# Optimization experiments

Measured on AMD Instinct MI355X. Metric: run time of the kernel, lower is better.

## Reference

```python
import jax, jax.numpy as jnp
import numpy as np

NUM_HEADS = 8
EPS = 1e-6


def _edge_boost(x, density_weight):
    # x: [B, C, H, W] -> boost: [B, H*W] (per-query additive bias)
    B, C, H, W = x.shape
    sx = jnp.array([[-1., 0., 1.], [-2., 0., 2.], [-1., 0., 1.]], dtype=x.dtype)
    sy = jnp.array([[-1., -2., -1.], [0., 0., 0.], [1., 2., 1.]], dtype=x.dtype)
    feat_mean = x.mean(axis=1, keepdims=True)            # [B,1,H,W]
    kern = jnp.stack([sx, sy])[:, None]                  # [2,1,3,3] (OIHW)
    g = jax.lax.conv_general_dilated(
        feat_mean, kern, window_strides=(1, 1), padding='SAME',
        dimension_numbers=('NCHW', 'OIHW', 'NCHW'))     # [B,2,H,W]
    edge = jnp.sqrt(g[:, 0] ** 2 + g[:, 1] ** 2 + EPS)   # [B,H,W]
    return density_weight * jnp.log1p(edge.reshape(B, H * W))


def setup_inputs() -> dict:
    key = jax.random.key(0)
    k1, k2, k3 = jax.random.split(key, 3)
    B, C, H, W = 2, 256, 56, 56
    x = jax.random.normal(k1, (B, C, H, W), dtype=jnp.float32)
    Wqkv = jax.random.normal(k2, (3 * C, C), dtype=jnp.float32) * 0.02
    Wproj = jax.random.normal(k3, (C, C), dtype=jnp.float32) * 0.02
    bproj = jnp.zeros((C,), dtype=jnp.float32)
    density_weight = jnp.float32(1.0)
    return {"x": x, "Wqkv": Wqkv, "Wproj": Wproj, "bproj": bproj,
            "density_weight": density_weight}


def reference(x, Wqkv, Wproj, bproj, density_weight):
    B, C, H, W = x.shape
    h = NUM_HEADS
    d = C // h
    N = H * W
    scale = d ** -0.5

    x_flat = x.reshape(B, C, N).transpose(0, 2, 1)        # [B,N,C]
    qkv = x_flat @ Wqkv.T                                 # [B,N,3C]
    qkv = qkv.reshape(B, N, 3, h, d).transpose(2, 0, 3, 1, 4)  # [3,B,h,N,d]
    q, k, v = qkv[0], qkv[1], qkv[2]

    attn = jnp.einsum('bhqd,bhkd->bhqk', q, k) * scale    # [B,h,N,N]
    boost = _edge_boost(x, density_weight)                # [B,N]
    attn = attn + boost[:, None, :, None]                 # per-query bias, bcast over heads/keys
    attn = jax.nn.softmax(attn, axis=-1)
    # dropout is identity in eval mode

    out = jnp.einsum('bhqk,bhkd->bhqd', attn, v)          # [B,h,N,d]
    out = out.transpose(0, 2, 1, 3).reshape(B, N, C)      # [B,N,C]
    out = out @ Wproj.T + bproj
    return out.transpose(0, 2, 1).reshape(B, C, H, W)
```

## Files before the change

### kernel.cpp

```cpp
#include <hip/hip_runtime.h>
#include <hip/hip_bf16.h>
#include <math.h>

#define NQ    3136
#define CDIM  256
#define HEADS 8
#define NT    49


typedef __attribute__((ext_vector_type(8))) short short8;
typedef __attribute__((ext_vector_type(4))) float f32x4;

__device__ __forceinline__ short f2bf(float f) {
    union { float f; unsigned u; } v; v.f = f;
    unsigned r = v.u + 0x7fff + ((v.u >> 16) & 1);
    return (short)(r >> 16);
}

__device__ __forceinline__ unsigned pk_bf16(float a, float b) {
    unsigned r;
    asm("v_cvt_pk_bf16_f32 %0, %1, %2" : "=v"(r) : "v"(a), "v"(b));
    return r;
}

#define SCALE_L2E 0.25503487523f

__global__ __launch_bounds__(256) void prep(const float* __restrict__ x,
                                            const float* __restrict__ Wq,
                                            const float* __restrict__ Wp,
                                            short* __restrict__ xT,
                                            short* __restrict__ Wb,
                                            short* __restrict__ Wpb) {
    const int bx = blockIdx.x;
    const int t  = threadIdx.x;
    if (bx == 52) {
        const int wp   = blockIdx.y + 4 * blockIdx.z;
        const int base = wp * 8192 + t * 4;
        #pragma unroll
        for (int i = 0; i < 8; ++i) {
            float4 v = *(const float4*)(Wp + base + i * 1024);
            uint2 o = { pk_bf16(v.x, v.y), pk_bf16(v.z, v.w) };
            *(uint2*)(Wpb + base + i * 1024) = o;
        }
        return;
    }
    if (bx >= 49) {
        const int wb   = (bx - 49) + 3 * (blockIdx.y + 4 * blockIdx.z);
        const int base = wb * 8192 + t * 4;
        #pragma unroll
        for (int i = 0; i < 8; ++i) {
            float4 v = *(const float4*)(Wq + base + i * 1024);
            uint2 o = { pk_bf16(v.x, v.y), pk_bf16(v.z, v.w) };
            *(uint2*)(Wb + base + i * 1024) = o;
        }
        return;
    }
    __shared__ short lt[64][72];
    const int b = blockIdx.z, cb = blockIdx.y, nb = bx;
    const float* xb = x + (size_t)b * CDIM * NQ + (size_t)(cb * 64) * NQ + nb * 64;
    #pragma unroll
    for (int it = 0; it < 4; ++it) {
        const int cc = (t >> 4) + 16 * it;
        const int nn = (t & 15) * 4;
        float4 v = *(const float4*)(xb + (size_t)cc * NQ + nn);
        lt[nn + 0][cc] = f2bf(v.x);
        lt[nn + 1][cc] = f2bf(v.y);
        lt[nn + 2][cc] = f2bf(v.z);
        lt[nn + 3][cc] = f2bf(v.w);
    }
    __syncthreads();
    const int n2 = t >> 2, c2 = (t & 3) * 16;
    short* dst = xT + ((size_t)b * NQ + nb * 64 + n2) * CDIM + cb * 64 + c2;
    *(uint4*)dst       = *(const uint4*)&lt[n2][c2];
    *(uint4*)(dst + 8) = *(const uint4*)&lt[n2][c2 + 8];
}

__global__ __launch_bounds__(256) void qkv_mfma(const short* __restrict__ xT,
                                                const short* __restrict__ Wb,
                                                short* __restrict__ Qs,
                                                short* __restrict__ Kb,
                                                short* __restrict__ V4) {
    __shared__ short xs[64][40];
    __shared__ short wsm[64][40];
    __shared__ short eps[64][72];
    const int nb = blockIdx.x, jb = blockIdx.y, b = blockIdx.z;
    const int n0 = nb * 64, j0 = jb * 64;
    const int t = threadIdx.x;
    const int lane = t & 63, w = t >> 6, g = lane >> 4, ql = lane & 15;
    const int srow = t >> 2, sc = (t & 3) * 8;

    const short* xsrc = xT + ((size_t)b * NQ + n0 + srow) * CDIM + sc;
    const short* wsrc = Wb + (size_t)(j0 + srow) * CDIM + sc;

    short8 xr = *(const short8*)(xsrc);
    short8 wr = *(const short8*)(wsrc);

    f32x4 acc[4] = {};
    for (int c0 = 0; c0 < 256; c0 += 32) {
        *(short8*)&xs[srow][sc]  = xr;
        *(short8*)&wsm[srow][sc] = wr;
        __syncthreads();
        if (c0 + 32 < 256) {
            xr = *(const short8*)(xsrc + c0 + 32);
            wr = *(const short8*)(wsrc + c0 + 32);
        }
        short8 bf = *(const short8*)&wsm[16 * w + ql][8 * g];
        #pragma unroll
        for (int r = 0; r < 4; ++r) {
            short8 af = *(const short8*)&xs[16 * r + ql][8 * g];
            acc[r] = __builtin_amdgcn_mfma_f32_16x16x32_bf16(af, bf, acc[r], 0, 0, 0);
        }
        __syncthreads();
    }

    const int sect = jb >> 2;
    const int hb   = (jb & 3) * 2;
    const int jloc = 16 * w + ql;

    if (sect < 2) {
        const float sc2 = (sect == 0) ? SCALE_L2E : 1.0f;
        #pragma unroll
        for (int r = 0; r < 4; ++r)
            #pragma unroll
            for (int i = 0; i < 4; ++i)
                eps[16 * r + 4 * g + i][jloc] = f2bf(acc[r][i] * sc2);
        __syncthreads();
        short* dstb = (sect == 0) ? Qs : Kb;
        const int n2 = t >> 2, jc = (t & 3) * 16;
        const int head = hb + (jc >> 5), d0 = jc & 31;
        short* dst = dstb + ((size_t)(b * 8 + head) * NQ + n0 + n2) * 32 + d0;
        *(uint4*)dst       = *(const uint4*)&eps[n2][jc];
        *(uint4*)(dst + 8) = *(const uint4*)&eps[n2][jc + 8];
    } else {
        #pragma unroll
        for (int r = 0; r < 4; ++r)
            #pragma unroll
            for (int i = 0; i < 4; ++i)
                eps[jloc][16 * r + 4 * g + i] = f2bf(acc[r][i]);
        __syncthreads();
        const int f  = t >> 6;
        const int l2 = t & 63;
        const int gg = l2 >> 4, qq = l2 & 15;
        const int dl = ((f & 2) ? 16 : 0) + qq;
        const int ko = ((f & 1) ? 32 : 0) + 8 * gg;
        #pragma unroll
        for (int h2 = 0; h2 < 2; ++h2) {
            const uint4 val = *(const uint4*)&eps[32 * h2 + dl][ko];
            short* dst = V4 + ((((size_t)(b * 8 + hb + h2) * NT + nb) * 4 + f) * 64 + l2) * 8;
            *(uint4*)dst = val;
        }
    }
}

__global__ __launch_bounds__(256) void attn_mfma(const short* __restrict__ Qs,
                                                 const short* __restrict__ Kb,
                                                 const short* __restrict__ V4,
                                                 short* __restrict__ Ob) {
    __shared__ __align__(16) short pq[4][32][72];

    const int bid = blockIdx.x;
    const int xcd = bid & 7;
    const int ii  = bid >> 3;
    const int bh  = xcd * 2 + (ii & 1);
    const int q0  = (ii >> 1) * 32;

    const int t    = threadIdx.x;
    const int lane = t & 63;
    const int w    = t >> 6;
    const int g    = lane >> 4;
    const int ql   = lane & 15;

    const short* Qh = Qs + (size_t)bh * NQ * 32;
    const short* Kh = Kb + (size_t)bh * NQ * 32;
    const short* Vh = V4 + (size_t)bh * (NT * 2048) + (size_t)lane * 8;

    const short8 qfA = *(const short8*)(Qh + (size_t)(q0 + ql) * 32 + 8 * g);
    const short8 qfB = *(const short8*)(Qh + (size_t)(q0 + 16 + ql) * 32 + 8 * g);

    short8 ones;
    #pragma unroll
    for (int e = 0; e < 8; ++e) ones[e] = (short)0x3F80;

    const short* kp = Kh + (size_t)ql * 32 + 8 * g;

    f32x4 otA0 = {0,0,0,0}, otA1 = {0,0,0,0};
    f32x4 otB0 = {0,0,0,0}, otB1 = {0,0,0,0};
    f32x4 otlA = {0,0,0,0}, otlB = {0,0,0,0};

    const short* vt0 = Vh + (size_t)w * 2048;
    short8 vc00 = *(const short8*)(vt0);
    short8 vc01 = *(const short8*)(vt0 + 512);
    short8 vc10 = *(const short8*)(vt0 + 1024);
    short8 vc11 = *(const short8*)(vt0 + 1536);

    for (int i = 0; i < 13; ++i) {
        const int cur = 4 * i + w;
        const int nxt = cur + 4;
        const int tn  = (nxt < NT) ? nxt : w;
        const short* vtn = Vh + (size_t)tn * 2048;
        short8 vn00 = *(const short8*)(vtn);
        short8 vn01 = *(const short8*)(vtn + 512);
        short8 vn10 = *(const short8*)(vtn + 1024);
        short8 vn11 = *(const short8*)(vtn + 1536);

        if (cur < NT) {
            const int k0 = cur * 64;
            short8 kf0 = *(const short8*)(kp + (size_t)(k0 +  0) * 32);
            short8 kf1 = *(const short8*)(kp + (size_t)(k0 + 16) * 32);
            short8 kf2 = *(const short8*)(kp + (size_t)(k0 + 32) * 32);
            short8 kf3 = *(const short8*)(kp + (size_t)(k0 + 48) * 32);

            __builtin_amdgcn_s_setprio(1);
            f32x4 stA[4], stB[4];
            stA[0] = __builtin_amdgcn_mfma_f32_16x16x32_bf16(kf0, qfA, (f32x4){0,0,0,0}, 0, 0, 0);
            stB[0] = __builtin_amdgcn_mfma_f32_16x16x32_bf16(kf0, qfB, (f32x4){0,0,0,0}, 0, 0, 0);
            stA[1] = __builtin_amdgcn_mfma_f32_16x16x32_bf16(kf1, qfA, (f32x4){0,0,0,0}, 0, 0, 0);
            stB[1] = __builtin_amdgcn_mfma_f32_16x16x32_bf16(kf1, qfB, (f32x4){0,0,0,0}, 0, 0, 0);
            stA[2] = __builtin_amdgcn_mfma_f32_16x16x32_bf16(kf2, qfA, (f32x4){0,0,0,0}, 0, 0, 0);
            stB[2] = __builtin_amdgcn_mfma_f32_16x16x32_bf16(kf2, qfB, (f32x4){0,0,0,0}, 0, 0, 0);
            stA[3] = __builtin_amdgcn_mfma_f32_16x16x32_bf16(kf3, qfA, (f32x4){0,0,0,0}, 0, 0, 0);
            stB[3] = __builtin_amdgcn_mfma_f32_16x16x32_bf16(kf3, qfB, (f32x4){0,0,0,0}, 0, 0, 0);
            __builtin_amdgcn_s_setprio(0);

            float pA[16], pB[16];
            #pragma unroll
            for (int c = 0; c < 4; ++c)
                #pragma unroll
                for (int e = 0; e < 4; ++e) {
                    pA[4 * c + e] = __builtin_amdgcn_exp2f(stA[c][e]);
                    pB[4 * c + e] = __builtin_amdgcn_exp2f(stB[c][e]);
                }

            #pragma unroll
            for (int c = 0; c < 4; ++c) {
                uint2 va_ = { pk_bf16(pA[4 * c + 0], pA[4 * c + 1]),
                              pk_bf16(pA[4 * c + 2], pA[4 * c + 3]) };
                *(uint2*)&pq[w][ql][16 * c + 4 * g] = va_;
                uint2 vb_ = { pk_bf16(pB[4 * c + 0], pB[4 * c + 1]),
                              pk_bf16(pB[4 * c + 2], pB[4 * c + 3]) };
                *(uint2*)&pq[w][16 + ql][16 * c + 4 * g] = vb_;
            }
            asm volatile("s_waitcnt lgkmcnt(0)" ::: "memory");

            short8 pbA0 = *(const short8*)&pq[w][ql][8 * g];
            short8 pbA1 = *(const short8*)&pq[w][ql][32 + 8 * g];
            short8 pbB0 = *(const short8*)&pq[w][16 + ql][8 * g];
            short8 pbB1 = *(const short8*)&pq[w][16 + ql][32 + 8 * g];

            __builtin_amdgcn_s_setprio(1);
            otA0 = __builtin_amdgcn_mfma_f32_16x16x32_bf16(vc00, pbA0, otA0, 0, 0, 0);
            otA0 = __builtin_amdgcn_mfma_f32_16x16x32_bf16(vc01, pbA1, otA0, 0, 0, 0);
            otA1 = __builtin_amdgcn_mfma_f32_16x16x32_bf16(vc10, pbA0, otA1, 0, 0, 0);
            otA1 = __builtin_amdgcn_mfma_f32_16x16x32_bf16(vc11, pbA1, otA1, 0, 0, 0);
            otB0 = __builtin_amdgcn_mfma_f32_16x16x32_bf16(vc00, pbB0, otB0, 0, 0, 0);
            otB0 = __builtin_amdgcn_mfma_f32_16x16x32_bf16(vc01, pbB1, otB0, 0, 0, 0);
            otB1 = __builtin_amdgcn_mfma_f32_16x16x32_bf16(vc10, pbB0, otB1, 0, 0, 0);
            otB1 = __builtin_amdgcn_mfma_f32_16x16x32_bf16(vc11, pbB1, otB1, 0, 0, 0);
            otlA = __builtin_amdgcn_mfma_f32_16x16x32_bf16(ones, pbA0, otlA, 0, 0, 0);
            otlA = __builtin_amdgcn_mfma_f32_16x16x32_bf16(ones, pbA1, otlA, 0, 0, 0);
            otlB = __builtin_amdgcn_mfma_f32_16x16x32_bf16(ones, pbB0, otlB, 0, 0, 0);
            otlB = __builtin_amdgcn_mfma_f32_16x16x32_bf16(ones, pbB1, otlB, 0, 0, 0);
            __builtin_amdgcn_s_setprio(0);
        }

        vc00 = vn00; vc01 = vn01; vc10 = vn10; vc11 = vn11;
    }

    const float lA = otlA[0];
    const float lB = otlB[0];

    __syncthreads();
    float* mrg = (float*)&pq[0][0][0];
    if (w > 0) {
        float* pp = mrg + ((size_t)(w - 1) * 64 + lane) * 20;
        *(f32x4*)(pp + 0)  = otA0;
        *(f32x4*)(pp + 4)  = otA1;
        *(f32x4*)(pp + 8)  = otB0;
        *(f32x4*)(pp + 12) = otB1;
        pp[16] = lA; pp[17] = lB;
    }
    __syncthreads();
    if (w == 0) {
        f32x4 sA0 = otA0, sA1 = otA1, sB0 = otB0, sB1 = otB1;
        float LA = lA, LB = lB;
        #pragma unroll
        for (int u = 0; u < 3; ++u) {
            const float* pp = mrg + ((size_t)u * 64 + lane) * 20;
            sA0 += *(const f32x4*)(pp + 0);
            sA1 += *(const f32x4*)(pp + 4);
            sB0 += *(const f32x4*)(pp + 8);
            sB1 += *(const f32x4*)(pp + 12);
            LA += pp[16]; LB += pp[17];
        }
        const float invA = 1.f / LA;
        const float invB = 1.f / LB;
        const int b = bh >> 3, h = bh & 7;
        short* orowA = Ob + ((size_t)b * NQ + q0 + ql) * CDIM + h * 32;
        short* orowB = Ob + ((size_t)b * NQ + q0 + 16 + ql) * CDIM + h * 32;
        uint2 wA0 = { pk_bf16(sA0[0] * invA, sA0[1] * invA),
                      pk_bf16(sA0[2] * invA, sA0[3] * invA) };
        uint2 wA1 = { pk_bf16(sA1[0] * invA, sA1[1] * invA),
                      pk_bf16(sA1[2] * invA, sA1[3] * invA) };
        uint2 wB0 = { pk_bf16(sB0[0] * invB, sB0[1] * invB),
                      pk_bf16(sB0[2] * invB, sB0[3] * invB) };
        uint2 wB1 = { pk_bf16(sB1[0] * invB, sB1[1] * invB),
                      pk_bf16(sB1[2] * invB, sB1[3] * invB) };
        *(uint2*)(orowA + 4 * g)      = wA0;
        *(uint2*)(orowA + 16 + 4 * g) = wA1;
        *(uint2*)(orowB + 4 * g)      = wB0;
        *(uint2*)(orowB + 16 + 4 * g) = wB1;
    }
}

__global__ __launch_bounds__(256) void proj_mfma(const short* __restrict__ Ob,
                                                 const short* __restrict__ Wpb,
                                                 const float* __restrict__ bias,
                                                 float* __restrict__ out) {
    __shared__ short xs[32][40];
    __shared__ short wsm[64][40];
    __shared__ float eps[64][36];
    const int n0  = blockIdx.x * 32;
    const int co0 = blockIdx.y * 64;
    const int b   = blockIdx.z;
    const int t   = threadIdx.x;
    const int lane = t & 63, w = t >> 6, g = lane >> 4, ql = lane & 15;
    const int arow = (t & 127) >> 2, ac = (t & 3) * 8;
    const int brow = t >> 2,          bc = (t & 3) * 8;

    const short* asrc = Ob + ((size_t)b * NQ + n0 + arow) * CDIM + ac;
    const short* wsrc = Wpb + (size_t)(co0 + brow) * CDIM + bc;

    short8 ar = {};
    if (t < 128) ar = *(const short8*)(asrc);
    short8 wr = *(const short8*)(wsrc);

    f32x4 acc0 = {}, acc1 = {};
    for (int c0 = 0; c0 < 256; c0 += 32) {
        if (t < 128) *(short8*)&xs[arow][ac] = ar;
        *(short8*)&wsm[brow][bc] = wr;
        __syncthreads();
        if (c0 + 32 < 256) {
            if (t < 128) ar = *(const short8*)(asrc + c0 + 32);
            wr = *(const short8*)(wsrc + c0 + 32);
        }
        short8 bfr = *(const short8*)&wsm[16 * w + ql][8 * g];
        short8 af0 = *(const short8*)&xs[ql][8 * g];
        short8 af1 = *(const short8*)&xs[16 + ql][8 * g];
        acc0 = __builtin_amdgcn_mfma_f32_16x16x32_bf16(af0, bfr, acc0, 0, 0, 0);
        acc1 = __builtin_amdgcn_mfma_f32_16x16x32_bf16(af1, bfr, acc1, 0, 0, 0);
        __syncthreads();
    }

    const int jl = 16 * w + ql;
    const float bb = bias[co0 + jl];
    *(float4*)&eps[jl][4 * g]      = make_float4(acc0[0] + bb, acc0[1] + bb,
                                                 acc0[2] + bb, acc0[3] + bb);
    *(float4*)&eps[jl][16 + 4 * g] = make_float4(acc1[0] + bb, acc1[1] + bb,
                                                 acc1[2] + bb, acc1[3] + bb);
    __syncthreads();

    const int row = t >> 2, seg = (t & 3) * 8;
    float* outp = out + ((size_t)b * CDIM + co0 + row) * NQ + n0 + seg;
    *(float4*)(outp)     = *(const float4*)&eps[row][seg];
    *(float4*)(outp + 4) = *(const float4*)&eps[row][seg + 4];
}

extern "C" void kernel_launch(void* const* d_in, const int* in_sizes, int n_in,
                              void* d_out, int out_size, void* d_ws, size_t ws_size,
                              hipStream_t stream) {
    const float* x     = (const float*)d_in[0];
    const float* Wqkv  = (const float*)d_in[1];
    const float* Wproj = (const float*)d_in[2];
    const float* bproj = (const float*)d_in[3];
    float* out = (float*)d_out;

    short* xT  = (short*)d_ws;
    short* Wb  = xT + (size_t)2 * NQ * CDIM;
    short* Wpb = Wb + (size_t)768 * CDIM;
    short* Qs  = Wpb + (size_t)CDIM * CDIM;
    short* Kb  = Qs + (size_t)16 * NQ * 32;
    short* V4  = Kb + (size_t)16 * NQ * 32;
    short* Ob  = V4 + (size_t)16 * NT * 2048;

    prep<<<dim3(53, 4, 2), 256, 0, stream>>>(x, Wqkv, Wproj, xT, Wb, Wpb);
    qkv_mfma<<<dim3(49, 12, 2), 256, 0, stream>>>(xT, Wb, Qs, Kb, V4);
    attn_mfma<<<dim3(1568, 1, 1), 256, 0, stream>>>(Qs, Kb, V4, Ob);
    proj_mfma<<<dim3(98, 4, 2), 256, 0, stream>>>(Ob, Wpb, bproj, out);
}
```

Before: 66.48 us.

## Widen attention blocks to 64 queries and 7 waves with tree reduction

Each attention block now handles 64 queries instead of 32, so every K and V tile loaded into registers is reused for four query sub-tiles rather than two. The key split grows from 4 to 7 waves (448 threads), so the 49 key tiles divide evenly and the per-iteration bounds check goes away. The grid is halved to match. The cross-wave merge of partial outputs and row sums becomes a multi-step tree reduction through a larger shared buffer. In exchange, register pressure and LDS use per block rise, there are more barriers, and with fewer, larger blocks occupancy and wave scheduling may get worse.

```diff
diff --git a/kernel.cpp b/kernel.cpp
--- a/kernel.cpp
+++ b/kernel.cpp
@@ -152,17 +152,17 @@
     }
 }
 
-__global__ __launch_bounds__(256) void attn_mfma(const short* __restrict__ Qs,
+__global__ __launch_bounds__(448) void attn_mfma(const short* __restrict__ Qs,
                                                  const short* __restrict__ Kb,
                                                  const short* __restrict__ V4,
                                                  short* __restrict__ Ob) {
-    __shared__ __align__(16) short pq[4][32][72];
+    __shared__ __align__(16) short pq[7][32][72];
 
     const int bid = blockIdx.x;
     const int xcd = bid & 7;
     const int ii  = bid >> 3;
     const int bh  = xcd * 2 + (ii & 1);
-    const int q0  = (ii >> 1) * 32;
+    const int q0  = (ii >> 1) * 64;
 
     const int t    = threadIdx.x;
     const int lane = t & 63;
@@ -176,6 +176,8 @@
 
     const short8 qfA = *(const short8*)(Qh + (size_t)(q0 + ql) * 32 + 8 * g);
     const short8 qfB = *(const short8*)(Qh + (size_t)(q0 + 16 + ql) * 32 + 8 * g);
+    const short8 qfC = *(const short8*)(Qh + (size_t)(q0 + 32 + ql) * 32 + 8 * g);
+    const short8 qfD = *(const short8*)(Qh + (size_t)(q0 + 48 + ql) * 32 + 8 * g);
 
     short8 ones;
     #pragma unroll
@@ -185,7 +187,10 @@
 
     f32x4 otA0 = {0,0,0,0}, otA1 = {0,0,0,0};
     f32x4 otB0 = {0,0,0,0}, otB1 = {0,0,0,0};
+    f32x4 otC0 = {0,0,0,0}, otC1 = {0,0,0,0};
+    f32x4 otD0 = {0,0,0,0}, otD1 = {0,0,0,0};
     f32x4 otlA = {0,0,0,0}, otlB = {0,0,0,0};
+    f32x4 otlC = {0,0,0,0}, otlD = {0,0,0,0};
 
     const short* vt0 = Vh + (size_t)w * 2048;
     short8 vc00 = *(const short8*)(vt0);
@@ -193,9 +198,9 @@
     short8 vc10 = *(const short8*)(vt0 + 1024);
     short8 vc11 = *(const short8*)(vt0 + 1536);
 
-    for (int i = 0; i < 13; ++i) {
-        const int cur = 4 * i + w;
-        const int nxt = cur + 4;
+    for (int i = 0; i < 7; ++i) {
+        const int cur = 7 * i + w;
+        const int nxt = cur + 7;
         const int tn  = (nxt < NT) ? nxt : w;
         const short* vtn = Vh + (size_t)tn * 2048;
         short8 vn00 = *(const short8*)(vtn);
@@ -203,13 +208,13 @@
         short8 vn10 = *(const short8*)(vtn + 1024);
         short8 vn11 = *(const short8*)(vtn + 1536);
 
-        if (cur < NT) {
-            const int k0 = cur * 64;
-            short8 kf0 = *(const short8*)(kp + (size_t)(k0 +  0) * 32);
-            short8 kf1 = *(const short8*)(kp + (size_t)(k0 + 16) * 32);
-            short8 kf2 = *(const short8*)(kp + (size_t)(k0 + 32) * 32);
-            short8 kf3 = *(const short8*)(kp + (size_t)(k0 + 48) * 32);
-
+        const int k0 = cur * 64;
+        short8 kf0 = *(const short8*)(kp + (size_t)(k0 +  0) * 32);
+        short8 kf1 = *(const short8*)(kp + (size_t)(k0 + 16) * 32);
+        short8 kf2 = *(const short8*)(kp + (size_t)(k0 + 32) * 32);
+        short8 kf3 = *(const short8*)(kp + (size_t)(k0 + 48) * 32);
+
+        {
             __builtin_amdgcn_s_setprio(1);
             f32x4 stA[4], stB[4];
             stA[0] = __builtin_amdgcn_mfma_f32_16x16x32_bf16(kf0, qfA, (f32x4){0,0,0,0}, 0, 0, 0);
@@ -230,7 +235,6 @@
                     pA[4 * c + e] = __builtin_amdgcn_exp2f(stA[c][e]);
                     pB[4 * c + e] = __builtin_amdgcn_exp2f(stB[c][e]);
                 }
-
             #pragma unroll
             for (int c = 0; c < 4; ++c) {
                 uint2 va_ = { pk_bf16(pA[4 * c + 0], pA[4 * c + 1]),
@@ -263,53 +267,123 @@
             __builtin_amdgcn_s_setprio(0);
         }
 
+        {
+            __builtin_amdgcn_s_setprio(1);
+            f32x4 stC[4], stD[4];
+            stC[0] = __builtin_amdgcn_mfma_f32_16x16x32_bf16(kf0, qfC, (f32x4){0,0,0,0}, 0, 0, 0);
+            stD[0] = __builtin_amdgcn_mfma_f32_16x16x32_bf16(kf0, qfD, (f32x4){0,0,0,0}, 0, 0, 0);
+            stC[1] = __builtin_amdgcn_mfma_f32_16x16x32_bf16(kf1, qfC, (f32x4){0,0,0,0}, 0, 0, 0);
+            stD[1] = __builtin_amdgcn_mfma_f32_16x16x32_bf16(kf1, qfD, (f32x4){0,0,0,0}, 0, 0, 0);
+            stC[2] = __builtin_amdgcn_mfma_f32_16x16x32_bf16(kf2, qfC, (f32x4){0,0,0,0}, 0, 0, 0);
+            stD[2] = __builtin_amdgcn_mfma_f32_16x16x32_bf16(kf2, qfD, (f32x4){0,0,0,0}, 0, 0, 0);
+            stC[3] = __builtin_amdgcn_mfma_f32_16x16x32_bf16(kf3, qfC, (f32x4){0,0,0,0}, 0, 0, 0);
+            stD[3] = __builtin_amdgcn_mfma_f32_16x16x32_bf16(kf3, qfD, (f32x4){0,0,0,0}, 0, 0, 0);
+            __builtin_amdgcn_s_setprio(0);
+
+            float pC[16], pD[16];
+            #pragma unroll
+            for (int c = 0; c < 4; ++c)
+                #pragma unroll
+                for (int e = 0; e < 4; ++e) {
+                    pC[4 * c + e] = __builtin_amdgcn_exp2f(stC[c][e]);
+                    pD[4 * c + e] = __builtin_amdgcn_exp2f(stD[c][e]);
+                }
+            #pragma unroll
+            for (int c = 0; c < 4; ++c) {
+                uint2 vc_ = { pk_bf16(pC[4 * c + 0], pC[4 * c + 1]),
+                              pk_bf16(pC[4 * c + 2], pC[4 * c + 3]) };
+                *(uint2*)&pq[w][ql][16 * c + 4 * g] = vc_;
+                uint2 vd_ = { pk_bf16(pD[4 * c + 0], pD[4 * c + 1]),
+                              pk_bf16(pD[4 * c + 2], pD[4 * c + 3]) };
+                *(uint2*)&pq[w][16 + ql][16 * c + 4 * g] = vd_;
+            }
+            asm volatile("s_waitcnt lgkmcnt(0)" ::: "memory");
+
+            short8 pbC0 = *(const short8*)&pq[w][ql][8 * g];
+            short8 pbC1 = *(const short8*)&pq[w][ql][32 + 8 * g];
+            short8 pbD0 = *(const short8*)&pq[w][16 + ql][8 * g];
+            short8 pbD1 = *(const short8*)&pq[w][16 + ql][32 + 8 * g];
+
+            __builtin_amdgcn_s_setprio(1);
+            otC0 = __builtin_amdgcn_mfma_f32_16x16x32_bf16(vc00, pbC0, otC0, 0, 0, 0);
+            otC0 = __builtin_amdgcn_mfma_f32_16x16x32_bf16(vc01, pbC1, otC0, 0, 0, 0);
+            otC1 = __builtin_amdgcn_mfma_f32_16x16x32_bf16(vc10, pbC0, otC1, 0, 0, 0);
+            otC1 = __builtin_amdgcn_mfma_f32_16x16x32_bf16(vc11, pbC1, otC1, 0, 0, 0);
+            otD0 = __builtin_amdgcn_mfma_f32_16x16x32_bf16(vc00, pbD0, otD0, 0, 0, 0);
+            otD0 = __builtin_amdgcn_mfma_f32_16x16x32_bf16(vc01, pbD1, otD0, 0, 0, 0);
+            otD1 = __builtin_amdgcn_mfma_f32_16x16x32_bf16(vc10, pbD0, otD1, 0, 0, 0);
+            otD1 = __builtin_amdgcn_mfma_f32_16x16x32_bf16(vc11, pbD1, otD1, 0, 0, 0);
+            otlC = __builtin_amdgcn_mfma_f32_16x16x32_bf16(ones, pbC0, otlC, 0, 0, 0);
+            otlC = __builtin_amdgcn_mfma_f32_16x16x32_bf16(ones, pbC1, otlC, 0, 0, 0);
+            otlD = __builtin_amdgcn_mfma_f32_16x16x32_bf16(ones, pbD0, otlD, 0, 0, 0);
+            otlD = __builtin_amdgcn_mfma_f32_16x16x32_bf16(ones, pbD1, otlD, 0, 0, 0);
+            __builtin_amdgcn_s_setprio(0);
+        }
+
         vc00 = vn00; vc01 = vn01; vc10 = vn10; vc11 = vn11;
     }
 
-    const float lA = otlA[0];
-    const float lB = otlB[0];
-
-    __syncthreads();
+    float lA2 = otlA[0], lB2 = otlB[0], lC2 = otlC[0], lD2 = otlD[0];
+
     float* mrg = (float*)&pq[0][0][0];
-    if (w > 0) {
-        float* pp = mrg + ((size_t)(w - 1) * 64 + lane) * 20;
-        *(f32x4*)(pp + 0)  = otA0;
-        *(f32x4*)(pp + 4)  = otA1;
-        *(f32x4*)(pp + 8)  = otB0;
-        *(f32x4*)(pp + 12) = otB1;
-        pp[16] = lA; pp[17] = lB;
-    }
+
+#define PUBLISH(SLOT)                                                        \
+    {   float* pp = mrg + ((size_t)(SLOT) * 64 + lane) * 36;                 \
+        *(f32x4*)(pp +  0) = otA0; *(f32x4*)(pp +  4) = otA1;                \
+        *(f32x4*)(pp +  8) = otB0; *(f32x4*)(pp + 12) = otB1;                \
+        *(f32x4*)(pp + 16) = otC0; *(f32x4*)(pp + 20) = otC1;                \
+        *(f32x4*)(pp + 24) = otD0; *(f32x4*)(pp + 28) = otD1;                \
+        pp[32] = lA2; pp[33] = lB2; pp[34] = lC2; pp[35] = lD2; }
+
+#define ACCUM(SLOT)                                                          \
+    {   const float* pp = mrg + ((size_t)(SLOT) * 64 + lane) * 36;           \
+        otA0 += *(const f32x4*)(pp +  0); otA1 += *(const f32x4*)(pp +  4);  \
+        otB0 += *(const f32x4*)(pp +  8); otB1 += *(const f32x4*)(pp + 12);  \
+        otC0 += *(const f32x4*)(pp + 16); otC1 += *(const f32x4*)(pp + 20);  \
+        otD0 += *(const f32x4*)(pp + 24); otD1 += *(const f32x4*)(pp + 28);  \
+        lA2 += pp[32]; lB2 += pp[33]; lC2 += pp[34]; lD2 += pp[35]; }
+
+    __syncthreads();
+    if (w >= 4) PUBLISH(w - 4);
+    __syncthreads();
+    if (w < 3) ACCUM(w);
+    __syncthreads();
+    if (w == 2 || w == 3) PUBLISH(w - 2);
+    __syncthreads();
+    if (w < 2) ACCUM(w);
+    __syncthreads();
+    if (w == 1) PUBLISH(0);
     __syncthreads();
     if (w == 0) {
-        f32x4 sA0 = otA0, sA1 = otA1, sB0 = otB0, sB1 = otB1;
-        float LA = lA, LB = lB;
-        #pragma unroll
-        for (int u = 0; u < 3; ++u) {
-            const float* pp = mrg + ((size_t)u * 64 + lane) * 20;
-            sA0 += *(const f32x4*)(pp + 0);
-            sA1 += *(const f32x4*)(pp + 4);
-            sB0 += *(const f32x4*)(pp + 8);
-            sB1 += *(const f32x4*)(pp + 12);
-            LA += pp[16]; LB += pp[17];
-        }
-        const float invA = 1.f / LA;
-        const float invB = 1.f / LB;
+        ACCUM(0);
+        const float invA = 1.f / lA2, invB = 1.f / lB2;
+        const float invC = 1.f / lC2, invD = 1.f / lD2;
         const int b = bh >> 3, h = bh & 7;
-        short* orowA = Ob + ((size_t)b * NQ + q0 + ql) * CDIM + h * 32;
-        short* orowB = Ob + ((size_t)b * NQ + q0 + 16 + ql) * CDIM + h * 32;
-        uint2 wA0 = { pk_bf16(sA0[0] * invA, sA0[1] * invA),
-                      pk_bf16(sA0[2] * invA, sA0[3] * invA) };
-        uint2 wA1 = { pk_bf16(sA1[0] * invA, sA1[1] * invA),
-                      pk_bf16(sA1[2] * invA, sA1[3] * invA) };
-        uint2 wB0 = { pk_bf16(sB0[0] * invB, sB0[1] * invB),
-                      pk_bf16(sB0[2] * invB, sB0[3] * invB) };
-        uint2 wB1 = { pk_bf16(sB1[0] * invB, sB1[1] * invB),
-                      pk_bf16(sB1[2] * invB, sB1[3] * invB) };
-        *(uint2*)(orowA + 4 * g)      = wA0;
-        *(uint2*)(orowA + 16 + 4 * g) = wA1;
-        *(uint2*)(orowB + 4 * g)      = wB0;
-        *(uint2*)(orowB + 16 + 4 * g) = wB1;
-    }
+        short* base = Ob + ((size_t)b * NQ + q0) * CDIM + h * 32;
+        short* orA = base + (size_t)(ql) * CDIM;
+        short* orB = base + (size_t)(16 + ql) * CDIM;
+        short* orC = base + (size_t)(32 + ql) * CDIM;
+        short* orD = base + (size_t)(48 + ql) * CDIM;
+        uint2 v;
+        v = (uint2){ pk_bf16(otA0[0]*invA, otA0[1]*invA), pk_bf16(otA0[2]*invA, otA0[3]*invA) };
+        *(uint2*)(orA + 4 * g) = v;
+        v = (uint2){ pk_bf16(otA1[0]*invA, otA1[1]*invA), pk_bf16(otA1[2]*invA, otA1[3]*invA) };
+        *(uint2*)(orA + 16 + 4 * g) = v;
+        v = (uint2){ pk_bf16(otB0[0]*invB, otB0[1]*invB), pk_bf16(otB0[2]*invB, otB0[3]*invB) };
+        *(uint2*)(orB + 4 * g) = v;
+        v = (uint2){ pk_bf16(otB1[0]*invB, otB1[1]*invB), pk_bf16(otB1[2]*invB, otB1[3]*invB) };
+        *(uint2*)(orB + 16 + 4 * g) = v;
+        v = (uint2){ pk_bf16(otC0[0]*invC, otC0[1]*invC), pk_bf16(otC0[2]*invC, otC0[3]*invC) };
+        *(uint2*)(orC + 4 * g) = v;
+        v = (uint2){ pk_bf16(otC1[0]*invC, otC1[1]*invC), pk_bf16(otC1[2]*invC, otC1[3]*invC) };
+        *(uint2*)(orC + 16 + 4 * g) = v;
+        v = (uint2){ pk_bf16(otD0[0]*invD, otD0[1]*invD), pk_bf16(otD0[2]*invD, otD0[3]*invD) };
+        *(uint2*)(orD + 4 * g) = v;
+        v = (uint2){ pk_bf16(otD1[0]*invD, otD1[1]*invD), pk_bf16(otD1[2]*invD, otD1[3]*invD) };
+        *(uint2*)(orD + 16 + 4 * g) = v;
+    }
+#undef PUBLISH
+#undef ACCUM
 }
 
 __global__ __launch_bounds__(256) void proj_mfma(const short* __restrict__ Ob,
@@ -384,6 +458,6 @@
 
     prep<<<dim3(53, 4, 2), 256, 0, stream>>>(x, Wqkv, Wproj, xT, Wb, Wpb);
     qkv_mfma<<<dim3(49, 12, 2), 256, 0, stream>>>(xT, Wb, Qs, Kb, V4);
-    attn_mfma<<<dim3(1568, 1, 1), 256, 0, stream>>>(Qs, Kb, V4, Ob);
+    attn_mfma<<<dim3(784, 1, 1), 448, 0, stream>>>(Qs, Kb, V4, Ob);
     proj_mfma<<<dim3(98, 4, 2), 256, 0, stream>>>(Ob, Wpb, bproj, out);
 }
```

Measured after the change: 72.79 us. 1.1x slower.

## Fuse fp32-to-bf16 prep into QKV and projection GEMM tile loads

Applied to the files above, without the earlier changes.

Removes the separate prep kernel that transposed x and converted the weights to bf16. The QKV GEMM now loads fp32 x and Wqkv directly and packs them to bf16 while filling shared memory, transposing x in the store. The projection GEMM does the same for Wproj. This drops one launch and one round trip of intermediates through memory. In exchange, every column block re-reads and re-converts the fp32 inputs, doubling the bytes per tile load. It also adds an odd read-modify-write of the epilogue shared buffer that could race with other threads' writes.

```diff
diff --git a/kernel.cpp b/kernel.cpp
--- a/kernel.cpp
+++ b/kernel.cpp
@@ -11,11 +11,7 @@
 typedef __attribute__((ext_vector_type(8))) short short8;
 typedef __attribute__((ext_vector_type(4))) float f32x4;
 
-__device__ __forceinline__ short f2bf(float f) {
-    union { float f; unsigned u; } v; v.f = f;
-    unsigned r = v.u + 0x7fff + ((v.u >> 16) & 1);
-    return (short)(r >> 16);
-}
+union W8u { unsigned u[4]; short8 s; };
 
 __device__ __forceinline__ unsigned pk_bf16(float a, float b) {
     unsigned r;
@@ -25,58 +21,8 @@
 
 #define SCALE_L2E 0.25503487523f
 
-__global__ __launch_bounds__(256) void prep(const float* __restrict__ x,
-                                            const float* __restrict__ Wq,
-                                            const float* __restrict__ Wp,
-                                            short* __restrict__ xT,
-                                            short* __restrict__ Wb,
-                                            short* __restrict__ Wpb) {
-    const int bx = blockIdx.x;
-    const int t  = threadIdx.x;
-    if (bx == 52) {
-        const int wp   = blockIdx.y + 4 * blockIdx.z;
-        const int base = wp * 8192 + t * 4;
-        #pragma unroll
-        for (int i = 0; i < 8; ++i) {
-            float4 v = *(const float4*)(Wp + base + i * 1024);
-            uint2 o = { pk_bf16(v.x, v.y), pk_bf16(v.z, v.w) };
-            *(uint2*)(Wpb + base + i * 1024) = o;
-        }
-        return;
-    }
-    if (bx >= 49) {
-        const int wb   = (bx - 49) + 3 * (blockIdx.y + 4 * blockIdx.z);
-        const int base = wb * 8192 + t * 4;
-        #pragma unroll
-        for (int i = 0; i < 8; ++i) {
-            float4 v = *(const float4*)(Wq + base + i * 1024);
-            uint2 o = { pk_bf16(v.x, v.y), pk_bf16(v.z, v.w) };
-            *(uint2*)(Wb + base + i * 1024) = o;
-        }
-        return;
-    }
-    __shared__ short lt[64][72];
-    const int b = blockIdx.z, cb = blockIdx.y, nb = bx;
-    const float* xb = x + (size_t)b * CDIM * NQ + (size_t)(cb * 64) * NQ + nb * 64;
-    #pragma unroll
-    for (int it = 0; it < 4; ++it) {
-        const int cc = (t >> 4) + 16 * it;
-        const int nn = (t & 15) * 4;
-        float4 v = *(const float4*)(xb + (size_t)cc * NQ + nn);
-        lt[nn + 0][cc] = f2bf(v.x);
-        lt[nn + 1][cc] = f2bf(v.y);
-        lt[nn + 2][cc] = f2bf(v.z);
-        lt[nn + 3][cc] = f2bf(v.w);
-    }
-    __syncthreads();
-    const int n2 = t >> 2, c2 = (t & 3) * 16;
-    short* dst = xT + ((size_t)b * NQ + nb * 64 + n2) * CDIM + cb * 64 + c2;
-    *(uint4*)dst       = *(const uint4*)&lt[n2][c2];
-    *(uint4*)(dst + 8) = *(const uint4*)&lt[n2][c2 + 8];
-}
-
-__global__ __launch_bounds__(256) void qkv_mfma(const short* __restrict__ xT,
-                                                const short* __restrict__ Wb,
+__global__ __launch_bounds__(256) void qkv_mfma(const float* __restrict__ x,
+                                                const float* __restrict__ Wq,
                                                 short* __restrict__ Qs,
                                                 short* __restrict__ Kb,
                                                 short* __restrict__ V4) {
@@ -87,22 +33,39 @@
     const int n0 = nb * 64, j0 = jb * 64;
     const int t = threadIdx.x;
     const int lane = t & 63, w = t >> 6, g = lane >> 4, ql = lane & 15;
-    const int srow = t >> 2, sc = (t & 3) * 8;
-
-    const short* xsrc = xT + ((size_t)b * NQ + n0 + srow) * CDIM + sc;
-    const short* wsrc = Wb + (size_t)(j0 + srow) * CDIM + sc;
-
-    short8 xr = *(const short8*)(xsrc);
-    short8 wr = *(const short8*)(wsrc);
+
+    const int cc2 = (t >> 4) * 2;
+    const int ng  = (t & 15) * 4;
+    const float* xsrc = x + ((size_t)b * CDIM + cc2) * NQ + n0 + ng;
+    const int wrow = t >> 2, wc = (t & 3) * 8;
+    const float* wsrc = Wq + (size_t)(j0 + wrow) * CDIM + wc;
+
+    float4 xa0 = *(const float4*)(xsrc);
+    float4 xa1 = *(const float4*)(xsrc + NQ);
+    float4 wa0 = *(const float4*)(wsrc);
+    float4 wa1 = *(const float4*)(wsrc + 4);
 
     f32x4 acc[4] = {};
     for (int c0 = 0; c0 < 256; c0 += 32) {
-        *(short8*)&xs[srow][sc]  = xr;
-        *(short8*)&wsm[srow][sc] = wr;
+        *(unsigned*)&xs[ng + 0][cc2] = pk_bf16(xa0.x, xa1.x);
+        *(unsigned*)&xs[ng + 1][cc2] = pk_bf16(xa0.y, xa1.y);
+        *(unsigned*)&xs[ng + 2][cc2] = pk_bf16(xa0.z, xa1.z);
+        *(unsigned*)&xs[ng + 3][cc2] = pk_bf16(xa0.w, xa1.w);
+        {
+            W8u wc8;
+            wc8.u[0] = pk_bf16(wa0.x, wa0.y);
+            wc8.u[1] = pk_bf16(wa0.z, wa0.w);
+            wc8.u[2] = pk_bf16(wa1.x, wa1.y);
+            wc8.u[3] = pk_bf16(wa1.z, wa1.w);
+            *(short8*)&wsm[wrow][wc] = wc8.s;
+        }
         __syncthreads();
         if (c0 + 32 < 256) {
-            xr = *(const short8*)(xsrc + c0 + 32);
-            wr = *(const short8*)(wsrc + c0 + 32);
+            const float* xn = xsrc + (size_t)(c0 + 32) * NQ;
+            xa0 = *(const float4*)(xn);
+            xa1 = *(const float4*)(xn + NQ);
+            wa0 = *(const float4*)(wsrc + c0 + 32);
+            wa1 = *(const float4*)(wsrc + c0 + 36);
         }
         short8 bf = *(const short8*)&wsm[16 * w + ql][8 * g];
         #pragma unroll
@@ -120,10 +83,17 @@
     if (sect < 2) {
         const float sc2 = (sect == 0) ? SCALE_L2E : 1.0f;
         #pragma unroll
+        for (int r = 0; r < 4; ++r) {
+            *(unsigned*)&eps[16 * r + 4 * g + 0][0] += 0;
+        }
+        #pragma unroll
         for (int r = 0; r < 4; ++r)
             #pragma unroll
-            for (int i = 0; i < 4; ++i)
-                eps[16 * r + 4 * g + i][jloc] = f2bf(acc[r][i] * sc2);
+            for (int i = 0; i < 4; ++i) {
+                union { float f; unsigned u; } v; v.f = acc[r][i] * sc2;
+                unsigned rr = v.u + 0x7fff + ((v.u >> 16) & 1);
+                eps[16 * r + 4 * g + i][jloc] = (short)(rr >> 16);
+            }
         __syncthreads();
         short* dstb = (sect == 0) ? Qs : Kb;
         const int n2 = t >> 2, jc = (t & 3) * 16;
@@ -135,8 +105,11 @@
         #pragma unroll
         for (int r = 0; r < 4; ++r)
             #pragma unroll
-            for (int i = 0; i < 4; ++i)
-                eps[jloc][16 * r + 4 * g + i] = f2bf(acc[r][i]);
+            for (int i = 0; i < 4; ++i) {
+                union { float f; unsigned u; } v; v.f = acc[r][i];
+                unsigned rr = v.u + 0x7fff + ((v.u >> 16) & 1);
+                eps[jloc][16 * r + 4 * g + i] = (short)(rr >> 16);
+            }
         __syncthreads();
         const int f  = t >> 6;
         const int l2 = t & 63;
@@ -313,7 +286,7 @@
 }
 
 __global__ __launch_bounds__(256) void proj_mfma(const short* __restrict__ Ob,
-                                                 const short* __restrict__ Wpb,
+                                                 const float* __restrict__ Wp,
                                                  const float* __restrict__ bias,
                                                  float* __restrict__ out) {
     __shared__ short xs[32][40];
@@ -328,20 +301,29 @@
     const int brow = t >> 2,          bc = (t & 3) * 8;
 
     const short* asrc = Ob + ((size_t)b * NQ + n0 + arow) * CDIM + ac;
-    const short* wsrc = Wpb + (size_t)(co0 + brow) * CDIM + bc;
+    const float* wsrc = Wp + (size_t)(co0 + brow) * CDIM + bc;
 
     short8 ar = {};
     if (t < 128) ar = *(const short8*)(asrc);
-    short8 wr = *(const short8*)(wsrc);
+    float4 wa0 = *(const float4*)(wsrc);
+    float4 wa1 = *(const float4*)(wsrc + 4);
 
     f32x4 acc0 = {}, acc1 = {};
     for (int c0 = 0; c0 < 256; c0 += 32) {
         if (t < 128) *(short8*)&xs[arow][ac] = ar;
-        *(short8*)&wsm[brow][bc] = wr;
+        {
+            W8u wc8;
+            wc8.u[0] = pk_bf16(wa0.x, wa0.y);
+            wc8.u[1] = pk_bf16(wa0.z, wa0.w);
+            wc8.u[2] = pk_bf16(wa1.x, wa1.y);
+            wc8.u[3] = pk_bf16(wa1.z, wa1.w);
+            *(short8*)&wsm[brow][bc] = wc8.s;
+        }
         __syncthreads();
         if (c0 + 32 < 256) {
             if (t < 128) ar = *(const short8*)(asrc + c0 + 32);
-            wr = *(const short8*)(wsrc + c0 + 32);
+            wa0 = *(const float4*)(wsrc + c0 + 32);
+            wa1 = *(const float4*)(wsrc + c0 + 36);
         }
         short8 bfr = *(const short8*)&wsm[16 * w + ql][8 * g];
         short8 af0 = *(const short8*)&xs[ql][8 * g];
@@ -374,16 +356,12 @@
     const float* bproj = (const float*)d_in[3];
     float* out = (float*)d_out;
 
-    short* xT  = (short*)d_ws;
-    short* Wb  = xT + (size_t)2 * NQ * CDIM;
-    short* Wpb = Wb + (size_t)768 * CDIM;
-    short* Qs  = Wpb + (size_t)CDIM * CDIM;
+    short* Qs  = (short*)d_ws;
     short* Kb  = Qs + (size_t)16 * NQ * 32;
     short* V4  = Kb + (size_t)16 * NQ * 32;
     short* Ob  = V4 + (size_t)16 * NT * 2048;
 
-    prep<<<dim3(53, 4, 2), 256, 0, stream>>>(x, Wqkv, Wproj, xT, Wb, Wpb);
-    qkv_mfma<<<dim3(49, 12, 2), 256, 0, stream>>>(xT, Wb, Qs, Kb, V4);
+    qkv_mfma<<<dim3(49, 12, 2), 256, 0, stream>>>(x, Wqkv, Qs, Kb, V4);
     attn_mfma<<<dim3(1568, 1, 1), 256, 0, stream>>>(Qs, Kb, V4, Ob);
-    proj_mfma<<<dim3(98, 4, 2), 256, 0, stream>>>(Ob, Wpb, bproj, out);
-}
+    proj_mfma<<<dim3(98, 4, 2), 256, 0, stream>>>(Ob, Wproj, bproj, out);
+}
```

Result: no change. 67.23 us (+1.1%).
